# Optimization experiments

Hardware: AMD Instinct MI355X
Metric: run time of the kernel (lower is better)

The kernel has to match this reference:

```python
import jax, jax.numpy as jnp
import numpy as np
import math

HIDDEN = 128; NHEADS = 4; N_COE = 50; N_SCALES = 4; THRE = 5.0; S = 4096; B = 1


def setup_inputs():
    key = jax.random.key(0)
    ks = jax.random.split(key, 12)
    w = lambda k, shape: jax.random.normal(k, shape, jnp.float32) * 0.05
    return {
        "eigenvalue": jax.random.uniform(ks[0], (B, S), jnp.float32) * 2.0,  # graph Laplacian eigvals in [0,2)
        "length": jnp.full((B,), S, dtype=jnp.int32),
        "sele_num": jnp.full((B,), S, dtype=jnp.int32),
        "eig_w_W": w(ks[1], (HIDDEN + 1, HIDDEN)), "eig_w_b": jnp.zeros((HIDDEN,), jnp.float32),
        "mha_ln_g": jnp.ones((HIDDEN,), jnp.float32), "mha_ln_b": jnp.zeros((HIDDEN,), jnp.float32),
        "in_W": w(ks[2], (HIDDEN, 3 * HIDDEN)), "in_b": jnp.zeros((3 * HIDDEN,), jnp.float32),
        "out_W": w(ks[3], (HIDDEN, HIDDEN)), "out_b": jnp.zeros((HIDDEN,), jnp.float32),
        "ffn_ln_g": jnp.ones((HIDDEN,), jnp.float32), "ffn_ln_b": jnp.zeros((HIDDEN,), jnp.float32),
        "ffn1_W": w(ks[4], (HIDDEN, HIDDEN)), "ffn1_b": jnp.zeros((HIDDEN,), jnp.float32),
        "ffn2_W": w(ks[5], (HIDDEN, HIDDEN)), "ffn2_b": jnp.zeros((HIDDEN,), jnp.float32),
        "dsc_W": w(ks[6], (HIDDEN, N_COE)), "dsc_b": jnp.zeros((N_COE,), jnp.float32),
        "dwv_W": w(ks[7], (HIDDEN, N_COE)), "dwv_b": jnp.zeros((N_COE,), jnp.float32),
        "dss_W": w(ks[8], (HIDDEN, N_SCALES)), "dss_b": jnp.zeros((N_SCALES,), jnp.float32),
    }


def layer_norm(x, g, b, eps=1e-5):
    m = x.mean(-1, keepdims=True)
    v = ((x - m) ** 2).mean(-1, keepdims=True)
    return (x - m) / jnp.sqrt(v + eps) * g + b


def sine_encoding(e, W, b):
    # e: [B, S] -> [B, S, HIDDEN]
    div = jnp.exp(jnp.arange(0, HIDDEN, 2, dtype=e.dtype) * (-math.log(10000.0) / HIDDEN))
    pe = (e * 100.0)[..., None] * div  # [B, S, HIDDEN/2]
    eeig = jnp.concatenate([e[..., None], jnp.sin(pe), jnp.cos(pe)], axis=-1)  # [B, S, HIDDEN+1]
    return eeig @ W + b


def mha(x, pad_mask, in_W, in_b, out_W, out_b):
    # x: [B, S, D]; pad_mask: [B, S] True = masked key
    Bb, Ss, D = x.shape
    hd = D // NHEADS
    qkv = x @ in_W + in_b
    q, k, v = jnp.split(qkv, 3, axis=-1)
    hsplit = lambda t: t.reshape(Bb, Ss, NHEADS, hd).transpose(0, 2, 1, 3)  # [B, H, S, hd]
    q, k, v = hsplit(q), hsplit(k), hsplit(v)
    scores = jnp.einsum('bhqd,bhkd->bhqk', q, k) / math.sqrt(hd)
    scores = jnp.where(pad_mask[:, None, None, :], -jnp.inf, scores)
    attn = jax.nn.softmax(scores, axis=-1)
    o = jnp.einsum('bhqk,bhkd->bhqd', attn, v).transpose(0, 2, 1, 3).reshape(Bb, Ss, D)
    return o @ out_W + out_b


def cheb_base(y, n_coe, flag):
    # Chebyshev recurrence: wavelet = [T_0, T_2, ...], scaling = [T_1, T_3, ...]
    te0 = jnp.ones_like(y)
    to0 = y
    def step(carry, _):
        te, to = carry
        te = 2.0 * y * to - te
        to = 2.0 * y * te - to
        return (te, to), (te, to)
    _, (evens, odds) = jax.lax.scan(step, (te0, to0), None, length=n_coe - 1)
    if flag == 'scaling':
        base = jnp.concatenate([to0[None], odds], axis=0)   # [n_coe, B, S, d]
    else:
        base = jnp.concatenate([te0[None], evens], axis=0)
    return jnp.moveaxis(base, 0, 1)  # [B, n_coe, S, d]


def _forward(eigenvalue, eig_w_W, eig_w_b, mha_ln_g, mha_ln_b, in_W, in_b, out_W, out_b,
             ffn_ln_g, ffn_ln_b, ffn1_W, ffn1_b, ffn2_W, ffn2_b,
             dsc_W, dsc_b, dwv_W, dwv_b, dss_W, dss_b, length, sele_num):
    Bb, Ss = eigenvalue.shape
    eve = eigenvalue
    eig_mask = jnp.arange(Ss)[None, :] >= sele_num[:, None]  # [B, S] True = pad
    # --- EigenEncoding (dropout in eval mode = identity) ---
    eig = sine_encoding(eve, eig_w_W, eig_w_b)
    eig = eig + mha(layer_norm(eig, mha_ln_g, mha_ln_b), eig_mask, in_W, in_b, out_W, out_b)
    f = layer_norm(eig, ffn_ln_g, ffn_ln_b)
    f = jax.nn.gelu(f @ ffn1_W + ffn1_b, approximate=False) @ ffn2_W + ffn2_b
    eig_filter = eig + f  # [B, S, HIDDEN]
    lenf = length.astype(eve.dtype)[:, None]
    def pooled(W, b):
        c = eig_filter @ W + b
        c = jnp.where(eig_mask[..., None], 0.0, c)
        return c.sum(axis=1) / (lenf + 1e-8)
    coe_scaling = jax.nn.sigmoid(pooled(dsc_W, dsc_b))
    coe_scaling = coe_scaling / (coe_scaling.sum(-1, keepdims=True) + 1e-8)  # [B, n_coe]
    coe_wavelet = jax.nn.sigmoid(pooled(dwv_W, dwv_b))
    coe_wavelet = coe_wavelet / (coe_wavelet.sum(-1, keepdims=True) + 1e-8)
    coe_scales = jax.nn.sigmoid(pooled(dss_W, dss_b)) * THRE  # [B, n_scales]
    # --- Chebyshev bases ---
    base_scaling = cheb_base(eve[..., None] - 1.0, N_COE, 'scaling')  # [B, n_coe, S, 1]
    fsw = eve[..., None] * coe_scales[:, None, :]                      # [B, S, n_scales]
    fsw = jnp.where(fsw > 2.0, 0.0, fsw)
    base_wavelet = cheb_base(fsw - 1.0, N_COE, 'wavelet')             # [B, n_coe, S, n_scales]
    base_scaling = 0.5 * (1.0 - base_scaling)
    base_wavelet = 0.5 * (1.0 - base_wavelet)
    curr_scaling = jnp.einsum('bc,bcsd->bsd', coe_scaling, base_scaling)
    curr_wavelet = jnp.einsum('bc,bcsd->bsd', coe_wavelet, base_wavelet)
    out = jnp.concatenate([curr_scaling, curr_wavelet], axis=-1)       # [B, S, 1+n_scales]
    out = out / (jnp.linalg.norm(out, axis=-1, keepdims=True) + 1e-8)  # cfg.lam.tight_use = True
    return out


def reference(eigenvalue, length, sele_num, eig_w_W, eig_w_b, mha_ln_g, mha_ln_b, in_W, in_b,
              out_W, out_b, ffn_ln_g, ffn_ln_b, ffn1_W, ffn1_b, ffn2_W, ffn2_b,
              dsc_W, dsc_b, dwv_W, dwv_b, dss_W, dss_b):
    return _forward(eigenvalue, eig_w_W, eig_w_b, mha_ln_g, mha_ln_b, in_W, in_b, out_W, out_b,
                    ffn_ln_g, ffn_ln_b, ffn1_W, ffn1_b, ffn2_W, ffn2_b,
                    dsc_W, dsc_b, dwv_W, dwv_b, dss_W, dss_b, length, sele_num)
```

## Files before the change

kernel.cpp:

```cpp
#include <hip/hip_runtime.h>
#include <math.h>


#define KSPLIT 4

typedef __attribute__((ext_vector_type(8))) short short8;
typedef __attribute__((ext_vector_type(4))) short short4v;
typedef __attribute__((ext_vector_type(4))) float f32x4;

__device__ inline unsigned short f2bf(float x) {
    unsigned u = __float_as_uint(x);
    return (unsigned short)((u + 0x7FFFu + ((u >> 16) & 1u)) >> 16);
}
__device__ inline float bf2f(unsigned short h) { return __uint_as_float(((unsigned)h) << 16); }

__global__ __launch_bounds__(256) void k_eig(const float* __restrict__ eve,
    const float* __restrict__ W, const float* __restrict__ bias,
    float* __restrict__ eig)
{
    __shared__ __align__(16) float se[8][132];
    const int t = threadIdx.x;
    const int r0 = blockIdx.x * 8;
    {
        const int r = t >> 5, l = t & 31;
        const float e = eve[r0 + r];
        if (l == 0) se[r][128] = e;
        const float e100 = e * 100.0f;
        #pragma unroll
        for (int jj = 0; jj < 2; ++jj) {
            const int j = l * 2 + jj;
            const float div = __expf(-0.07195578415606394f * (float)(2 * j));
            const float pe = e100 * div;
            se[r][j]      = __sinf(pe);
            se[r][64 + j] = __cosf(pe);
        }
    }
    __syncthreads();
    const int c = t & 127;
    const int rg = t >> 7;
    float acc[4];
    {
        const float w0 = W[c];
        #pragma unroll
        for (int i = 0; i < 4; ++i) acc[i] = se[rg + 2 * i][128] * w0;
    }
    #pragma unroll 8
    for (int k = 0; k < 128; k += 4) {
        const float w0 = W[(k + 1) * 128 + c];
        const float w1 = W[(k + 2) * 128 + c];
        const float w2 = W[(k + 3) * 128 + c];
        const float w3 = W[(k + 4) * 128 + c];
        #pragma unroll
        for (int i = 0; i < 4; ++i) {
            const float4 x = *(const float4*)&se[rg + 2 * i][k];
            float a = acc[i];
            a = fmaf(x.x, w0, a);
            a = fmaf(x.y, w1, a);
            a = fmaf(x.z, w2, a);
            a = fmaf(x.w, w3, a);
            acc[i] = a;
        }
    }
    const float bb = bias[c];
    #pragma unroll
    for (int i = 0; i < 4; ++i) eig[(r0 + rg + 2 * i) * 128 + c] = acc[i] + bb;
}

__global__ __launch_bounds__(256) void k_qkv(const float* __restrict__ eig,
    const float* __restrict__ g, const float* __restrict__ b,
    const float* __restrict__ inW, const float* __restrict__ inb,
    float* __restrict__ qkv, unsigned short* __restrict__ Khi_g,
    unsigned short* __restrict__ Klo_g, unsigned short* __restrict__ Vt_g)
{
    __shared__ __align__(16) float xn[8][128];
    __shared__ float red1[8][32];
    __shared__ float red2[8][32];
    __shared__ __align__(16) unsigned short vsh[128][8];
    const int t = threadIdx.x;
    const int r0 = blockIdx.x * 8;
    const int r = t >> 5, l = t & 31;
    float v[4];
    {
        float s = 0.f, ss = 0.f;
        #pragma unroll
        for (int m = 0; m < 4; ++m) {
            const float x = eig[(r0 + r) * 128 + l + 32 * m];
            v[m] = x; s += x; ss += x * x;
        }
        red1[r][l] = s; red2[r][l] = ss;
    }
    __syncthreads();
    for (int o = 16; o > 0; o >>= 1) {
        if (l < o) { red1[r][l] += red1[r][l + o]; red2[r][l] += red2[r][l + o]; }
        __syncthreads();
    }
    {
        const float mean = red1[r][0] * (1.f / 128.f);
        const float var  = red2[r][0] * (1.f / 128.f) - mean * mean;
        const float inv  = 1.f / sqrtf(var + 1e-5f);
        #pragma unroll
        for (int m = 0; m < 4; ++m) {
            const int col = l + 32 * m;
            xn[r][col] = (v[m] - mean) * inv * g[col] + b[col];
        }
    }
    __syncthreads();
    const int cbase = t & 127;
    const int rg = t >> 7;
    float acc[3][4];
    #pragma unroll
    for (int p = 0; p < 3; ++p) {
        const float bb = inb[p * 128 + cbase];
        #pragma unroll
        for (int i = 0; i < 4; ++i) acc[p][i] = bb;
    }
    #pragma unroll 4
    for (int k = 0; k < 128; k += 4) {
        float4 xv[4];
        #pragma unroll
        for (int i = 0; i < 4; ++i) xv[i] = *(const float4*)&xn[rg + 2 * i][k];
        #pragma unroll
        for (int p = 0; p < 3; ++p) {
            const int c = p * 128 + cbase;
            const float w0 = inW[(k + 0) * 384 + c];
            const float w1 = inW[(k + 1) * 384 + c];
            const float w2 = inW[(k + 2) * 384 + c];
            const float w3 = inW[(k + 3) * 384 + c];
            #pragma unroll
            for (int i = 0; i < 4; ++i) {
                float a = acc[p][i];
                a = fmaf(xv[i].x, w0, a);
                a = fmaf(xv[i].y, w1, a);
                a = fmaf(xv[i].z, w2, a);
                a = fmaf(xv[i].w, w3, a);
                acc[p][i] = a;
            }
        }
    }
    #pragma unroll
    for (int i = 0; i < 4; ++i)
        qkv[(r0 + rg + 2 * i) * 384 + cbase] = acc[0][i];
    {
        const int h = cbase >> 5, d = cbase & 31;
        #pragma unroll
        for (int i = 0; i < 4; ++i) {
            const int row = r0 + rg + 2 * i;
            const float kv = acc[1][i];
            const unsigned short hb = f2bf(kv);
            Khi_g[((size_t)h * 4096 + row) * 32 + d] = hb;
            Klo_g[((size_t)h * 4096 + row) * 32 + d] = f2bf(kv - bf2f(hb));
        }
    }
    #pragma unroll
    for (int i = 0; i < 4; ++i)
        vsh[cbase][rg + 2 * i] = f2bf(acc[2][i]);
    __syncthreads();
    if (t < 128) {
        const uint4 vv = *(const uint4*)&vsh[t][0];
        *(uint4*)&Vt_g[(size_t)t * 4096 + r0] = vv;
    }
}

#define KSTR 40
#define VSTR 72
#define PSTR 72

__global__ __launch_bounds__(256) void k_attn(const float* __restrict__ qkv,
    const unsigned short* __restrict__ Khi_g, const unsigned short* __restrict__ Klo_g,
    const unsigned short* __restrict__ Vt_g,
    const int* __restrict__ sele, float* __restrict__ Oe, float* __restrict__ E)
{
    __shared__ __align__(16) unsigned short Khi[64 * KSTR];
    __shared__ __align__(16) unsigned short Klo[64 * KSTR];
    __shared__ __align__(16) unsigned short Vt[32 * VSTR];
    __shared__ __align__(16) unsigned short Pb[4][16 * PSTR];

    const int t = threadIdx.x;
    const int lane = t & 63;
    const int l = lane & 15;
    const int quad = lane >> 4;
    const int wv = __builtin_amdgcn_readfirstlane(t >> 6);
    const int qb = blockIdx.x;
    const int h  = blockIdx.y;
    const int ks = blockIdx.z;
    const int nk = sele[0];

    short8 qhi, qlo;
    {
        const float* __restrict__ qr = qkv + (size_t)(qb * 64 + wv * 16 + l) * 384 + h * 32 + quad * 8;
        const float4 a = *(const float4*)qr;
        const float4 b = *(const float4*)(qr + 4);
        const float sc = 0.17677669529663687f;
        float v[8] = {a.x * sc, a.y * sc, a.z * sc, a.w * sc, b.x * sc, b.y * sc, b.z * sc, b.w * sc};
        #pragma unroll
        for (int j = 0; j < 8; ++j) {
            const unsigned short hb = f2bf(v[j]);
            qhi[j] = (short)hb;
            qlo[j] = (short)f2bf(v[j] - bf2f(hb));
        }
    }
    f32x4 accO0 = {0.f, 0.f, 0.f, 0.f};
    f32x4 accO1 = {0.f, 0.f, 0.f, 0.f};
    float elane = 0.f;

    const int kk = t >> 2;
    const int d0 = (t & 3) * 8;
    const int vd = t >> 3;
    const int ko = (t & 7) * 8;

    for (int ch = 0; ch < 16; ++ch) {
        const int keybase = ks * 1024 + ch * 64;
        __syncthreads();
        {
            const uint4 kh16 = *(const uint4*)&Khi_g[((size_t)h * 4096 + keybase + kk) * 32 + d0];
            const uint4 kl16 = *(const uint4*)&Klo_g[((size_t)h * 4096 + keybase + kk) * 32 + d0];
            const uint4 vv16 = *(const uint4*)&Vt_g[((size_t)h * 32 + vd) * 4096 + keybase + ko];
            *(uint4*)&Khi[kk * KSTR + d0] = kh16;
            *(uint4*)&Klo[kk * KSTR + d0] = kl16;
            *(uint4*)&Vt[vd * VSTR + ko]  = vv16;
        }
        __syncthreads();
        unsigned short* __restrict__ Pw = Pb[wv];
        #pragma unroll
        for (int tile = 0; tile < 4; ++tile) {
            const int kl = tile * 16 + l;
            const short8 kh = *(const short8*)&Khi[kl * KSTR + quad * 8];
            const short8 kw = *(const short8*)&Klo[kl * KSTR + quad * 8];
            f32x4 S = {0.f, 0.f, 0.f, 0.f};
            S = __builtin_amdgcn_mfma_f32_16x16x32_bf16(kh, qhi, S, 0, 0, 0);
            S = __builtin_amdgcn_mfma_f32_16x16x32_bf16(kw, qhi, S, 0, 0, 0);
            S = __builtin_amdgcn_mfma_f32_16x16x32_bf16(kh, qlo, S, 0, 0, 0);
            const int kg0 = keybase + tile * 16 + quad * 4;
            short4v pw;
            #pragma unroll
            for (int r = 0; r < 4; ++r) {
                const float p = (kg0 + r < nk) ? __expf(S[r]) : 0.f;
                elane += p;
                pw[r] = (short)f2bf(p);
            }
            *(short4v*)&Pw[l * PSTR + tile * 16 + quad * 4] = pw;
        }
        #pragma unroll
        for (int step = 0; step < 2; ++step) {
            const short8 pa  = *(const short8*)&Pw[l * PSTR + step * 32 + quad * 8];
            const short8 vb0 = *(const short8*)&Vt[l * VSTR + step * 32 + quad * 8];
            const short8 vb1 = *(const short8*)&Vt[(16 + l) * VSTR + step * 32 + quad * 8];
            accO0 = __builtin_amdgcn_mfma_f32_16x16x32_bf16(pa, vb0, accO0, 0, 0, 0);
            accO1 = __builtin_amdgcn_mfma_f32_16x16x32_bf16(pa, vb1, accO1, 0, 0, 0);
        }
    }
    elane += __shfl_xor(elane, 16, 64);
    elane += __shfl_xor(elane, 32, 64);
    const int qrow0 = qb * 64 + wv * 16;
    if (lane < 16)
        E[((size_t)ks * 4 + h) * 4096 + qrow0 + l] = elane;
    #pragma unroll
    for (int r = 0; r < 4; ++r) {
        const size_t row = qrow0 + quad * 4 + r;
        Oe[((size_t)ks * 4096 + row) * 128 + h * 32 + l]      = accO0[r];
        Oe[((size_t)ks * 4096 + row) * 128 + h * 32 + 16 + l] = accO1[r];
    }
}

__global__ __launch_bounds__(256) void k_ffn(const float* __restrict__ eig,
    const float* __restrict__ Oe, const float* __restrict__ E,
    const float* __restrict__ outW, const float* __restrict__ outb,
    const float* __restrict__ lg, const float* __restrict__ lb,
    const float* __restrict__ W1, const float* __restrict__ b1,
    const float* __restrict__ W2, const float* __restrict__ b2,
    const int* __restrict__ sele, float* __restrict__ xsum)
{
    __shared__ __align__(16) float sA[8][128];
    __shared__ __align__(16) float x2[8][128];
    __shared__ __align__(16) float xn[8][128];
    __shared__ float red1[8][32];
    __shared__ float red2[8][32];
    __shared__ float sEr[8][4];
    __shared__ float colsum[2][128];
    const int t = threadIdx.x;
    const int r0 = blockIdx.x * 8;
    const int r = t >> 5, l = t & 31;
    if (l < 4) {
        float es = 0.f;
        #pragma unroll
        for (int ks = 0; ks < KSPLIT; ++ks)
            es += E[((size_t)ks * 4 + l) * 4096 + r0 + r];
        sEr[r][l] = 1.f / es;
    }
    __syncthreads();
    #pragma unroll
    for (int m = 0; m < 4; ++m) {
        const int col = l + 32 * m;
        float v = 0.f;
        #pragma unroll
        for (int ks = 0; ks < KSPLIT; ++ks)
            v += Oe[((size_t)ks * 4096 + r0 + r) * 128 + col];
        sA[r][col] = v * sEr[r][col >> 5];
    }
    __syncthreads();
    const int c = t & 127;
    const int rg = t >> 7;
    {
        float acc[4];
        const float bb = outb[c];
        #pragma unroll
        for (int i = 0; i < 4; ++i) acc[i] = bb;
        #pragma unroll 8
        for (int k = 0; k < 128; k += 4) {
            const float w0 = outW[(k + 0) * 128 + c];
            const float w1 = outW[(k + 1) * 128 + c];
            const float w2 = outW[(k + 2) * 128 + c];
            const float w3 = outW[(k + 3) * 128 + c];
            #pragma unroll
            for (int i = 0; i < 4; ++i) {
                const float4 x = *(const float4*)&sA[rg + 2 * i][k];
                float a = acc[i];
                a = fmaf(x.x, w0, a);
                a = fmaf(x.y, w1, a);
                a = fmaf(x.z, w2, a);
                a = fmaf(x.w, w3, a);
                acc[i] = a;
            }
        }
        #pragma unroll
        for (int i = 0; i < 4; ++i)
            x2[rg + 2 * i][c] = eig[(r0 + rg + 2 * i) * 128 + c] + acc[i];
    }
    __syncthreads();
    {
        float s = 0.f, ss = 0.f;
        float v[4];
        #pragma unroll
        for (int m = 0; m < 4; ++m) {
            const float x = x2[r][l + 32 * m];
            v[m] = x; s += x; ss += x * x;
        }
        red1[r][l] = s; red2[r][l] = ss;
        __syncthreads();
        for (int o = 16; o > 0; o >>= 1) {
            if (l < o) { red1[r][l] += red1[r][l + o]; red2[r][l] += red2[r][l + o]; }
            __syncthreads();
        }
        const float mean = red1[r][0] * (1.f / 128.f);
        const float var  = red2[r][0] * (1.f / 128.f) - mean * mean;
        const float inv  = 1.f / sqrtf(var + 1e-5f);
        #pragma unroll
        for (int m = 0; m < 4; ++m) {
            const int col = l + 32 * m;
            xn[r][col] = (v[m] - mean) * inv * lg[col] + lb[col];
        }
    }
    __syncthreads();
    {
        float acc[4];
        const float bb = b1[c];
        #pragma unroll
        for (int i = 0; i < 4; ++i) acc[i] = bb;
        #pragma unroll 8
        for (int k = 0; k < 128; k += 4) {
            const float w0 = W1[(k + 0) * 128 + c];
            const float w1 = W1[(k + 1) * 128 + c];
            const float w2 = W1[(k + 2) * 128 + c];
            const float w3 = W1[(k + 3) * 128 + c];
            #pragma unroll
            for (int i = 0; i < 4; ++i) {
                const float4 x = *(const float4*)&xn[rg + 2 * i][k];
                float a = acc[i];
                a = fmaf(x.x, w0, a);
                a = fmaf(x.y, w1, a);
                a = fmaf(x.z, w2, a);
                a = fmaf(x.w, w3, a);
                acc[i] = a;
            }
        }
        __syncthreads();
        #pragma unroll
        for (int i = 0; i < 4; ++i) {
            const float x = acc[i];
            sA[rg + 2 * i][c] = 0.5f * x * (1.f + erff(x * 0.70710678118654752f));
        }
    }
    __syncthreads();
    {
        float acc[4];
        const float bb = b2[c];
        #pragma unroll
        for (int i = 0; i < 4; ++i) acc[i] = bb;
        #pragma unroll 8
        for (int k = 0; k < 128; k += 4) {
            const float w0 = W2[(k + 0) * 128 + c];
            const float w1 = W2[(k + 1) * 128 + c];
            const float w2 = W2[(k + 2) * 128 + c];
            const float w3 = W2[(k + 3) * 128 + c];
            #pragma unroll
            for (int i = 0; i < 4; ++i) {
                const float4 x = *(const float4*)&sA[rg + 2 * i][k];
                float a = acc[i];
                a = fmaf(x.x, w0, a);
                a = fmaf(x.y, w1, a);
                a = fmaf(x.z, w2, a);
                a = fmaf(x.w, w3, a);
                acc[i] = a;
            }
        }
        const int nsel = sele[0];
        float local = 0.f;
        #pragma unroll
        for (int i = 0; i < 4; ++i) {
            const float ef = x2[rg + 2 * i][c] + acc[i];
            if (r0 + rg + 2 * i < nsel) local += ef;
        }
        colsum[rg][c] = local;
    }
    __syncthreads();
    if (rg == 0) atomicAdd(&xsum[c], colsum[0][c] + colsum[1][c]);
}

__global__ __launch_bounds__(128) void k_coef(const float* __restrict__ xsum,
    const float* __restrict__ dscW, const float* __restrict__ dscb,
    const float* __restrict__ dwvW, const float* __restrict__ dwvb,
    const float* __restrict__ dssW, const float* __restrict__ dssb,
    const int* __restrict__ len, const int* __restrict__ sele,
    float* __restrict__ coef)
{
    __shared__ float xs[128];
    __shared__ float csc[50], cwv[50];
    __shared__ float s2[2];
    const int t = threadIdx.x;
    xs[t] = xsum[t];
    __syncthreads();
    const float invl = 1.f / ((float)len[0] + 1e-8f);
    const float ns = (float)sele[0];
    if (t < 50) {
        float a = ns * dscb[t];
        for (int k = 0; k < 128; ++k) a = fmaf(xs[k], dscW[k * 50 + t], a);
        a *= invl;
        csc[t] = 1.f / (1.f + expf(-a));
    } else if (t >= 64 && t < 114) {
        const int j = t - 64;
        float a = ns * dwvb[j];
        for (int k = 0; k < 128; ++k) a = fmaf(xs[k], dwvW[k * 50 + j], a);
        a *= invl;
        cwv[j] = 1.f / (1.f + expf(-a));
    } else if (t >= 114 && t < 118) {
        const int j = t - 114;
        float a = ns * dssb[j];
        for (int k = 0; k < 128; ++k) a = fmaf(xs[k], dssW[k * 4 + j], a);
        a *= invl;
        coef[100 + j] = (1.f / (1.f + expf(-a))) * 5.0f;
    }
    __syncthreads();
    if (t == 0) { float s = 0.f; for (int i2 = 0; i2 < 50; ++i2) s += csc[i2]; s2[0] = s; }
    if (t == 1) { float s = 0.f; for (int i2 = 0; i2 < 50; ++i2) s += cwv[i2]; s2[1] = s; }
    __syncthreads();
    if (t < 50) {
        coef[t]      = csc[t] / (s2[0] + 1e-8f);
        coef[50 + t] = cwv[t] / (s2[1] + 1e-8f);
    }
}

__global__ __launch_bounds__(256) void k_out(const float* __restrict__ eve,
    const float* __restrict__ coef, float* __restrict__ out)
{
    __shared__ float csc[50], cwv[50], cs[4];
    const int t = threadIdx.x;
    if (t < 50) csc[t] = coef[t];
    else if (t < 100) cwv[t - 50] = coef[t];
    else if (t < 104) cs[t - 100] = coef[t];
    __syncthreads();
    const int s = blockIdx.x * 256 + t;
    const float e = eve[s];
    float vals[5];
    {
        const float y = e - 1.f;
        float te = 1.f, to = y;
        float a = csc[0] * (0.5f * (1.f - to));
        const float y2 = 2.f * y;
        for (int i = 1; i < 50; ++i) {
            te = fmaf(y2, to, -te);
            to = fmaf(y2, te, -to);
            a = fmaf(csc[i], 0.5f * (1.f - to), a);
        }
        vals[0] = a;
    }
    #pragma unroll
    for (int j = 0; j < 4; ++j) {
        float f = e * cs[j];
        if (f > 2.f) f = 0.f;
        const float y = f - 1.f;
        float te = 1.f, to = y;
        float a = cwv[0] * (0.5f * (1.f - te));
        const float y2 = 2.f * y;
        for (int i = 1; i < 50; ++i) {
            te = fmaf(y2, to, -te);
            to = fmaf(y2, te, -to);
            a = fmaf(cwv[i], 0.5f * (1.f - te), a);
        }
        vals[1 + j] = a;
    }
    float n2 = 0.f;
    #pragma unroll
    for (int k = 0; k < 5; ++k) n2 += vals[k] * vals[k];
    const float invn = 1.f / (sqrtf(n2) + 1e-8f);
    #pragma unroll
    for (int k = 0; k < 5; ++k) out[s * 5 + k] = vals[k] * invn;
}

extern "C" void kernel_launch(void* const* d_in, const int* in_sizes, int n_in,
                              void* d_out, int out_size, void* d_ws, size_t ws_size,
                              hipStream_t stream) {
    const float* eve  = (const float*)d_in[0];
    const int*   len  = (const int*)d_in[1];
    const int*   sele = (const int*)d_in[2];
    const float* eigW = (const float*)d_in[3];
    const float* eigB = (const float*)d_in[4];
    const float* mlg  = (const float*)d_in[5];
    const float* mlb  = (const float*)d_in[6];
    const float* inW  = (const float*)d_in[7];
    const float* inb  = (const float*)d_in[8];
    const float* outW = (const float*)d_in[9];
    const float* outb = (const float*)d_in[10];
    const float* flg  = (const float*)d_in[11];
    const float* flb  = (const float*)d_in[12];
    const float* W1   = (const float*)d_in[13];
    const float* b1   = (const float*)d_in[14];
    const float* W2   = (const float*)d_in[15];
    const float* b2   = (const float*)d_in[16];
    const float* dscW = (const float*)d_in[17];
    const float* dscb = (const float*)d_in[18];
    const float* dwvW = (const float*)d_in[19];
    const float* dwvb = (const float*)d_in[20];
    const float* dssW = (const float*)d_in[21];
    const float* dssb = (const float*)d_in[22];

    float* ws   = (float*)d_ws;
    float* eig  = ws;
    float* qkv  = ws + 524288;
    float* Oe   = ws + 2097152;
    float* E    = ws + 4194304;
    float* xsum = ws + 4259840;
    float* coef = ws + 4259968;
    unsigned short* Khi_g = (unsigned short*)(ws + 4260352);
    unsigned short* Klo_g = (unsigned short*)(ws + 4522496);
    unsigned short* Vt_g  = (unsigned short*)(ws + 4784640);
    float* out  = (float*)d_out;

    hipMemsetAsync(xsum, 0, 128 * sizeof(float), stream);
    k_eig <<<512, 256, 0, stream>>>(eve, eigW, eigB, eig);
    k_qkv <<<512, 256, 0, stream>>>(eig, mlg, mlb, inW, inb, qkv, Khi_g, Klo_g, Vt_g);
    k_attn<<<dim3(64, 4, KSPLIT), 256, 0, stream>>>(qkv, Khi_g, Klo_g, Vt_g, sele, Oe, E);
    k_ffn <<<512, 256, 0, stream>>>(eig, Oe, E, outW, outb, flg, flb, W1, b1, W2, b2, sele, xsum);
    k_coef<<<1, 128, 0, stream>>>(xsum, dscW, dscb, dwvW, dwvb, dssW, dssb, len, sele, coef);
    k_out <<<16, 256, 0, stream>>>(eve, coef, out);
}
```

Baseline: 207.6 us.

## Fuse eigen-encoding with QKV projection and pre-transpose weights for float4 loads

Merges the sine-encoding projection and the layernorm+QKV kernel into one kernel, so the encoded rows stay in shared memory instead of being written and read back. A new prep kernel transposes all dense weight matrices each call so per-thread weight reads become contiguous float4 loads along K. The trade-off is one extra launch plus a weight transpose on every call, and transposed reads are strided across threads (each thread reads its own 512-byte row), which may hurt coalescing. It also adds unroll pragmas in the coefficient kernel.

```diff
diff --git a/kernel.cpp b/kernel.cpp
--- a/kernel.cpp
+++ b/kernel.cpp
@@ -14,11 +14,47 @@
 }
 __device__ inline float bf2f(unsigned short h) { return __uint_as_float(((unsigned)h) << 16); }
 
-__global__ __launch_bounds__(256) void k_eig(const float* __restrict__ eve,
-    const float* __restrict__ W, const float* __restrict__ bias,
-    float* __restrict__ eig)
+__global__ __launch_bounds__(256) void k_wprep(const float* __restrict__ eigW,
+    const float* __restrict__ inW, const float* __restrict__ outW,
+    const float* __restrict__ W1, const float* __restrict__ W2,
+    float* __restrict__ eT0, float* __restrict__ eT, float* __restrict__ iT,
+    float* __restrict__ oT, float* __restrict__ w1T, float* __restrict__ w2T)
+{
+    const int i = blockIdx.x * 256 + threadIdx.x;
+    if (i < 16384) {
+        const int j = i & 127, c = i >> 7;
+        eT[c * 128 + j] = eigW[(j + 1) * 128 + c];
+    } else if (i < 65536) {
+        const int a = i - 16384;
+        const int k = a & 127, c = a >> 7;
+        iT[c * 128 + k] = inW[k * 384 + c];
+    } else if (i < 81920) {
+        const int a = i - 65536; const int k = a & 127, c = a >> 7;
+        oT[c * 128 + k] = outW[k * 128 + c];
+    } else if (i < 98304) {
+        const int a = i - 81920; const int k = a & 127, c = a >> 7;
+        w1T[c * 128 + k] = W1[k * 128 + c];
+    } else if (i < 114688) {
+        const int a = i - 98304; const int k = a & 127, c = a >> 7;
+        w2T[c * 128 + k] = W2[k * 128 + c];
+    } else if (i < 114816) {
+        eT0[i - 114688] = eigW[i - 114688];
+    }
+}
+
+__global__ __launch_bounds__(256) void k_embed(const float* __restrict__ eve,
+    const float* __restrict__ eT0, const float* __restrict__ eT, const float* __restrict__ ebias,
+    const float* __restrict__ g, const float* __restrict__ b,
+    const float* __restrict__ iT, const float* __restrict__ inb,
+    float* __restrict__ eig, float* __restrict__ qkv, unsigned short* __restrict__ Khi_g,
+    unsigned short* __restrict__ Klo_g, unsigned short* __restrict__ Vt_g)
 {
     __shared__ __align__(16) float se[8][132];
+    __shared__ __align__(16) float x[8][128];
+    __shared__ __align__(16) float xn[8][128];
+    __shared__ float red1[8][32];
+    __shared__ float red2[8][32];
+    __shared__ __align__(16) unsigned short vsh[128][8];
     const int t = threadIdx.x;
     const int r0 = blockIdx.x * 8;
     {
@@ -38,63 +74,49 @@
     __syncthreads();
     const int c = t & 127;
     const int rg = t >> 7;
-    float acc[4];
-    {
-        const float w0 = W[c];
+    {
+        float acc[4];
+        const float w0 = eT0[c];
         #pragma unroll
         for (int i = 0; i < 4; ++i) acc[i] = se[rg + 2 * i][128] * w0;
-    }
-    #pragma unroll 8
-    for (int k = 0; k < 128; k += 4) {
-        const float w0 = W[(k + 1) * 128 + c];
-        const float w1 = W[(k + 2) * 128 + c];
-        const float w2 = W[(k + 3) * 128 + c];
-        const float w3 = W[(k + 4) * 128 + c];
+        #pragma unroll 8
+        for (int k = 0; k < 128; k += 4) {
+            const float4 w = *(const float4*)&eT[c * 128 + k];
+            #pragma unroll
+            for (int i = 0; i < 4; ++i) {
+                const float4 xv = *(const float4*)&se[rg + 2 * i][k];
+                float a = acc[i];
+                a = fmaf(xv.x, w.x, a);
+                a = fmaf(xv.y, w.y, a);
+                a = fmaf(xv.z, w.z, a);
+                a = fmaf(xv.w, w.w, a);
+                acc[i] = a;
+            }
+        }
+        const float bb = ebias[c];
         #pragma unroll
         for (int i = 0; i < 4; ++i) {
-            const float4 x = *(const float4*)&se[rg + 2 * i][k];
-            float a = acc[i];
-            a = fmaf(x.x, w0, a);
-            a = fmaf(x.y, w1, a);
-            a = fmaf(x.z, w2, a);
-            a = fmaf(x.w, w3, a);
-            acc[i] = a;
-        }
-    }
-    const float bb = bias[c];
-    #pragma unroll
-    for (int i = 0; i < 4; ++i) eig[(r0 + rg + 2 * i) * 128 + c] = acc[i] + bb;
-}
-
-__global__ __launch_bounds__(256) void k_qkv(const float* __restrict__ eig,
-    const float* __restrict__ g, const float* __restrict__ b,
-    const float* __restrict__ inW, const float* __restrict__ inb,
-    float* __restrict__ qkv, unsigned short* __restrict__ Khi_g,
-    unsigned short* __restrict__ Klo_g, unsigned short* __restrict__ Vt_g)
-{
-    __shared__ __align__(16) float xn[8][128];
-    __shared__ float red1[8][32];
-    __shared__ float red2[8][32];
-    __shared__ __align__(16) unsigned short vsh[128][8];
-    const int t = threadIdx.x;
-    const int r0 = blockIdx.x * 8;
-    const int r = t >> 5, l = t & 31;
-    float v[4];
-    {
+            const float v = acc[i] + bb;
+            x[rg + 2 * i][c] = v;
+            eig[(r0 + rg + 2 * i) * 128 + c] = v;
+        }
+    }
+    __syncthreads();
+    {
+        const int r = t >> 5, l = t & 31;
+        float v[4];
         float s = 0.f, ss = 0.f;
         #pragma unroll
         for (int m = 0; m < 4; ++m) {
-            const float x = eig[(r0 + r) * 128 + l + 32 * m];
-            v[m] = x; s += x; ss += x * x;
+            const float xx = x[r][l + 32 * m];
+            v[m] = xx; s += xx; ss += xx * xx;
         }
         red1[r][l] = s; red2[r][l] = ss;
-    }
-    __syncthreads();
-    for (int o = 16; o > 0; o >>= 1) {
-        if (l < o) { red1[r][l] += red1[r][l + o]; red2[r][l] += red2[r][l + o]; }
         __syncthreads();
-    }
-    {
+        for (int o = 16; o > 0; o >>= 1) {
+            if (l < o) { red1[r][l] += red1[r][l + o]; red2[r][l] += red2[r][l + o]; }
+            __syncthreads();
+        }
         const float mean = red1[r][0] * (1.f / 128.f);
         const float var  = red2[r][0] * (1.f / 128.f) - mean * mean;
         const float inv  = 1.f / sqrtf(var + 1e-5f);
@@ -105,59 +127,55 @@
         }
     }
     __syncthreads();
-    const int cbase = t & 127;
-    const int rg = t >> 7;
-    float acc[3][4];
-    #pragma unroll
-    for (int p = 0; p < 3; ++p) {
-        const float bb = inb[p * 128 + cbase];
-        #pragma unroll
-        for (int i = 0; i < 4; ++i) acc[p][i] = bb;
-    }
-    #pragma unroll 4
-    for (int k = 0; k < 128; k += 4) {
-        float4 xv[4];
-        #pragma unroll
-        for (int i = 0; i < 4; ++i) xv[i] = *(const float4*)&xn[rg + 2 * i][k];
+    {
+        float acc[3][4];
         #pragma unroll
         for (int p = 0; p < 3; ++p) {
-            const int c = p * 128 + cbase;
-            const float w0 = inW[(k + 0) * 384 + c];
-            const float w1 = inW[(k + 1) * 384 + c];
-            const float w2 = inW[(k + 2) * 384 + c];
-            const float w3 = inW[(k + 3) * 384 + c];
+            const float bb = inb[p * 128 + c];
+            #pragma unroll
+            for (int i = 0; i < 4; ++i) acc[p][i] = bb;
+        }
+        #pragma unroll 4
+        for (int k = 0; k < 128; k += 4) {
+            float4 xv[4];
+            #pragma unroll
+            for (int i = 0; i < 4; ++i) xv[i] = *(const float4*)&xn[rg + 2 * i][k];
+            #pragma unroll
+            for (int p = 0; p < 3; ++p) {
+                const float4 w = *(const float4*)&iT[(p * 128 + c) * 128 + k];
+                #pragma unroll
+                for (int i = 0; i < 4; ++i) {
+                    float a = acc[p][i];
+                    a = fmaf(xv[i].x, w.x, a);
+                    a = fmaf(xv[i].y, w.y, a);
+                    a = fmaf(xv[i].z, w.z, a);
+                    a = fmaf(xv[i].w, w.w, a);
+                    acc[p][i] = a;
+                }
+            }
+        }
+        #pragma unroll
+        for (int i = 0; i < 4; ++i)
+            qkv[(r0 + rg + 2 * i) * 384 + c] = acc[0][i];
+        {
+            const int h = c >> 5, d = c & 31;
             #pragma unroll
             for (int i = 0; i < 4; ++i) {
-                float a = acc[p][i];
-                a = fmaf(xv[i].x, w0, a);
-                a = fmaf(xv[i].y, w1, a);
-                a = fmaf(xv[i].z, w2, a);
-                a = fmaf(xv[i].w, w3, a);
-                acc[p][i] = a;
-            }
-        }
-    }
-    #pragma unroll
-    for (int i = 0; i < 4; ++i)
-        qkv[(r0 + rg + 2 * i) * 384 + cbase] = acc[0][i];
-    {
-        const int h = cbase >> 5, d = cbase & 31;
-        #pragma unroll
-        for (int i = 0; i < 4; ++i) {
-            const int row = r0 + rg + 2 * i;
-            const float kv = acc[1][i];
-            const unsigned short hb = f2bf(kv);
-            Khi_g[((size_t)h * 4096 + row) * 32 + d] = hb;
-            Klo_g[((size_t)h * 4096 + row) * 32 + d] = f2bf(kv - bf2f(hb));
-        }
-    }
-    #pragma unroll
-    for (int i = 0; i < 4; ++i)
-        vsh[cbase][rg + 2 * i] = f2bf(acc[2][i]);
-    __syncthreads();
-    if (t < 128) {
-        const uint4 vv = *(const uint4*)&vsh[t][0];
-        *(uint4*)&Vt_g[(size_t)t * 4096 + r0] = vv;
+                const int row = r0 + rg + 2 * i;
+                const float kv = acc[1][i];
+                const unsigned short hb = f2bf(kv);
+                Khi_g[((size_t)h * 4096 + row) * 32 + d] = hb;
+                Klo_g[((size_t)h * 4096 + row) * 32 + d] = f2bf(kv - bf2f(hb));
+            }
+        }
+        #pragma unroll
+        for (int i = 0; i < 4; ++i)
+            vsh[c][rg + 2 * i] = f2bf(acc[2][i]);
+        __syncthreads();
+        if (t < 128) {
+            const uint4 vv = *(const uint4*)&vsh[t][0];
+            *(uint4*)&Vt_g[(size_t)t * 4096 + r0] = vv;
+        }
     }
 }
 
@@ -264,10 +282,10 @@
 
 __global__ __launch_bounds__(256) void k_ffn(const float* __restrict__ eig,
     const float* __restrict__ Oe, const float* __restrict__ E,
-    const float* __restrict__ outW, const float* __restrict__ outb,
+    const float* __restrict__ oT, const float* __restrict__ outb,
     const float* __restrict__ lg, const float* __restrict__ lb,
-    const float* __restrict__ W1, const float* __restrict__ b1,
-    const float* __restrict__ W2, const float* __restrict__ b2,
+    const float* __restrict__ w1T, const float* __restrict__ b1,
+    const float* __restrict__ w2T, const float* __restrict__ b2,
     const int* __restrict__ sele, float* __restrict__ xsum)
 {
     __shared__ __align__(16) float sA[8][128];
@@ -307,18 +325,15 @@
         for (int i = 0; i < 4; ++i) acc[i] = bb;
         #pragma unroll 8
         for (int k = 0; k < 128; k += 4) {
-            const float w0 = outW[(k + 0) * 128 + c];
-            const float w1 = outW[(k + 1) * 128 + c];
-            const float w2 = outW[(k + 2) * 128 + c];
-            const float w3 = outW[(k + 3) * 128 + c];
+            const float4 w = *(const float4*)&oT[c * 128 + k];
             #pragma unroll
             for (int i = 0; i < 4; ++i) {
                 const float4 x = *(const float4*)&sA[rg + 2 * i][k];
                 float a = acc[i];
-                a = fmaf(x.x, w0, a);
-                a = fmaf(x.y, w1, a);
-                a = fmaf(x.z, w2, a);
-                a = fmaf(x.w, w3, a);
+                a = fmaf(x.x, w.x, a);
+                a = fmaf(x.y, w.y, a);
+                a = fmaf(x.z, w.z, a);
+                a = fmaf(x.w, w.w, a);
                 acc[i] = a;
             }
         }
@@ -358,18 +373,15 @@
         for (int i = 0; i < 4; ++i) acc[i] = bb;
         #pragma unroll 8
         for (int k = 0; k < 128; k += 4) {
-            const float w0 = W1[(k + 0) * 128 + c];
-            const float w1 = W1[(k + 1) * 128 + c];
-            const float w2 = W1[(k + 2) * 128 + c];
-            const float w3 = W1[(k + 3) * 128 + c];
+            const float4 w = *(const float4*)&w1T[c * 128 + k];
             #pragma unroll
             for (int i = 0; i < 4; ++i) {
                 const float4 x = *(const float4*)&xn[rg + 2 * i][k];
                 float a = acc[i];
-                a = fmaf(x.x, w0, a);
-                a = fmaf(x.y, w1, a);
-                a = fmaf(x.z, w2, a);
-                a = fmaf(x.w, w3, a);
+                a = fmaf(x.x, w.x, a);
+                a = fmaf(x.y, w.y, a);
+                a = fmaf(x.z, w.z, a);
+                a = fmaf(x.w, w.w, a);
                 acc[i] = a;
             }
         }
@@ -388,18 +400,15 @@
         for (int i = 0; i < 4; ++i) acc[i] = bb;
         #pragma unroll 8
         for (int k = 0; k < 128; k += 4) {
-            const float w0 = W2[(k + 0) * 128 + c];
-            const float w1 = W2[(k + 1) * 128 + c];
-            const float w2 = W2[(k + 2) * 128 + c];
-            const float w3 = W2[(k + 3) * 128 + c];
+            const float4 w = *(const float4*)&w2T[c * 128 + k];
             #pragma unroll
             for (int i = 0; i < 4; ++i) {
                 const float4 x = *(const float4*)&sA[rg + 2 * i][k];
                 float a = acc[i];
-                a = fmaf(x.x, w0, a);
-                a = fmaf(x.y, w1, a);
-                a = fmaf(x.z, w2, a);
-                a = fmaf(x.w, w3, a);
+                a = fmaf(x.x, w.x, a);
+                a = fmaf(x.y, w.y, a);
+                a = fmaf(x.z, w.z, a);
+                a = fmaf(x.w, w.w, a);
                 acc[i] = a;
             }
         }
@@ -433,18 +442,21 @@
     const float ns = (float)sele[0];
     if (t < 50) {
         float a = ns * dscb[t];
+        #pragma unroll 8
         for (int k = 0; k < 128; ++k) a = fmaf(xs[k], dscW[k * 50 + t], a);
         a *= invl;
         csc[t] = 1.f / (1.f + expf(-a));
     } else if (t >= 64 && t < 114) {
         const int j = t - 64;
         float a = ns * dwvb[j];
+        #pragma unroll 8
         for (int k = 0; k < 128; ++k) a = fmaf(xs[k], dwvW[k * 50 + j], a);
         a *= invl;
         cwv[j] = 1.f / (1.f + expf(-a));
     } else if (t >= 114 && t < 118) {
         const int j = t - 114;
         float a = ns * dssb[j];
+        #pragma unroll 8
         for (int k = 0; k < 128; ++k) a = fmaf(xs[k], dssW[k * 4 + j], a);
         a *= invl;
         coef[100 + j] = (1.f / (1.f + expf(-a))) * 5.0f;
@@ -543,13 +555,20 @@
     unsigned short* Khi_g = (unsigned short*)(ws + 4260352);
     unsigned short* Klo_g = (unsigned short*)(ws + 4522496);
     unsigned short* Vt_g  = (unsigned short*)(ws + 4784640);
+    float* eT0  = ws + 5046784;
+    float* eT   = ws + 5046912;
+    float* iT   = ws + 5063296;
+    float* oT   = ws + 5112448;
+    float* w1T  = ws + 5128832;
+    float* w2T  = ws + 5145216;
     float* out  = (float*)d_out;
 
     hipMemsetAsync(xsum, 0, 128 * sizeof(float), stream);
-    k_eig <<<512, 256, 0, stream>>>(eve, eigW, eigB, eig);
-    k_qkv <<<512, 256, 0, stream>>>(eig, mlg, mlb, inW, inb, qkv, Khi_g, Klo_g, Vt_g);
-    k_attn<<<dim3(64, 4, KSPLIT), 256, 0, stream>>>(qkv, Khi_g, Klo_g, Vt_g, sele, Oe, E);
-    k_ffn <<<512, 256, 0, stream>>>(eig, Oe, E, outW, outb, flg, flb, W1, b1, W2, b2, sele, xsum);
-    k_coef<<<1, 128, 0, stream>>>(xsum, dscW, dscb, dwvW, dwvb, dssW, dssb, len, sele, coef);
-    k_out <<<16, 256, 0, stream>>>(eve, coef, out);
-}
+    k_wprep<<<449, 256, 0, stream>>>(eigW, inW, outW, W1, W2, eT0, eT, iT, oT, w1T, w2T);
+    k_embed<<<512, 256, 0, stream>>>(eve, eT0, eT, eigB, mlg, mlb, iT, inb,
+                                     eig, qkv, Khi_g, Klo_g, Vt_g);
+    k_attn <<<dim3(64, 4, KSPLIT), 256, 0, stream>>>(qkv, Khi_g, Klo_g, Vt_g, sele, Oe, E);
+    k_ffn  <<<512, 256, 0, stream>>>(eig, Oe, E, oT, outb, flg, flb, w1T, b1, w2T, b2, sele, xsum);
+    k_coef <<<1, 128, 0, stream>>>(xsum, dscW, dscb, dwvW, dwvb, dssW, dssb, len, sele, coef);
+    k_out  <<<16, 256, 0, stream>>>(eve, coef, out);
+}
```

After: 227.5 us. +9.6%, slower.
